# Optimization experiments

Measured on AMD Instinct MI355X. Metric: run time of the kernel, lower is better.

## Reference

```python
import jax, jax.numpy as jnp
import numpy as np

N, E, F_IN, H, C = 50000, 800000, 128, 4, 73
HC = H * C  # 292
NEG_SLOPE_ATT = 0.2   # GATv2 attention leaky relu
NEG_SLOPE_ACT = 0.01  # F.leaky_relu default
BN_EPS = 1e-5


def setup_inputs() -> dict:
    key = jax.random.key(0)
    ks = jax.random.split(key, 20)
    rn = lambda k, shp, s=0.05: (jax.random.normal(k, shp, jnp.float32) * s)
    inp = {
        'x': jax.random.normal(ks[0], (N, F_IN), jnp.float32),
        'edge_index': jax.random.randint(ks[1], (2, E), 0, N, jnp.int64),
        # conv1 (in=F_IN)
        'Wl1': rn(ks[2], (HC, F_IN)), 'bl1': rn(ks[3], (HC,)),
        'Wr1': rn(ks[4], (HC, F_IN)), 'br1': rn(ks[5], (HC,)),
        'att1': rn(ks[6], (H, C)), 'b1': rn(ks[7], (HC,)),
        # conv2 (in=HC)
        'Wl2': rn(ks[8], (HC, HC)), 'bl2': rn(ks[9], (HC,)),
        'Wr2': rn(ks[10], (HC, HC)), 'br2': rn(ks[11], (HC,)),
        'att2': rn(ks[12], (H, C)), 'b2': rn(ks[13], (HC,)),
        # shared BatchNorm1d(HC)
        'gamma': jnp.ones((HC,), jnp.float32), 'beta': jnp.zeros((HC,), jnp.float32),
        # classifier Linear(HC, 2)
        'Wc': rn(ks[14], (2, HC)), 'bc': rn(ks[15], (2,)),
    }
    return inp


def _gatv2(x, src, dst, Wl, bl, Wr, br, att, b):
    # lin_l on source, lin_r on target (PyG GATv2Conv, share_weights=False)
    xl = (x @ Wl.T + bl).reshape(-1, H, C)  # [N,H,C]
    xr = (x @ Wr.T + br).reshape(-1, H, C)
    f = xl[src] + xr[dst]                    # [E,H,C] edge-wise gather
    s = jnp.einsum('ehc,hc->eh', jax.nn.leaky_relu(f, NEG_SLOPE_ATT), att)
    # segment softmax over incoming edges of each destination node
    m = jax.ops.segment_max(s, dst, num_segments=N)
    ex = jnp.exp(s - m[dst])
    den = jax.ops.segment_sum(ex, dst, num_segments=N)
    alpha = ex / (den[dst] + 1e-16)          # [E,H]
    out = jax.ops.segment_sum(alpha[:, :, None] * xl[src], dst, num_segments=N)
    return out.reshape(-1, HC) + b           # concat heads + bias


def _bn(x, gamma, beta):
    mu = jnp.mean(x, axis=0)
    var = jnp.mean((x - mu) ** 2, axis=0)
    return (x - mu) * jax.lax.rsqrt(var + BN_EPS) * gamma + beta


def reference(x, edge_index, Wl1, bl1, Wr1, br1, att1, b1,
              Wl2, bl2, Wr2, br2, att2, b2, gamma, beta, Wc, bc):
    src, dst = edge_index[0], edge_index[1]
    h = _gatv2(x, src, dst, Wl1, bl1, Wr1, br1, att1, b1)
    h = jax.nn.leaky_relu(_bn(h, gamma, beta), NEG_SLOPE_ACT)
    h = _gatv2(h, src, dst, Wl2, bl2, Wr2, br2, att2, b2)
    h = jax.nn.leaky_relu(_bn(h, gamma, beta), NEG_SLOPE_ACT)
    return h @ Wc.T + bc
```

## Files before the change

### kernel.cpp

```cpp
#include <hip/hip_runtime.h>

#define HCDIM 292
#define NHEAD 4
#define CDIM 73
#define SLOTS 5
#define NPERM 320
#define BN_EPS 1e-5f
#define LOG2E 1.44269504f

using u16x8 = __attribute__((ext_vector_type(8))) unsigned short;
using f32x4 = __attribute__((ext_vector_type(4))) float;
using u16x4 = __attribute__((ext_vector_type(4))) unsigned short;
using hf2   = __attribute__((ext_vector_type(2))) _Float16;
using v2h   = __attribute__((ext_vector_type(2))) __fp16;
using v8h   = __attribute__((ext_vector_type(8))) __fp16;

__device__ inline v2h pkrtz(float a, float b) {
  return __builtin_amdgcn_cvt_pkrtz(a, b);
}
__device__ inline float fdot2(hf2 a, hf2 b, float c) {
  return __builtin_amdgcn_fdot2(__builtin_bit_cast(v2h, a),
                                __builtin_bit_cast(v2h, b), c, false);
}
__device__ inline ushort f2h(float f) {
  _Float16 h = (_Float16)f;
  return __builtin_bit_cast(ushort, h);
}
__device__ inline float h2f(ushort v) {
  return (float)__builtin_bit_cast(_Float16, v);
}
__device__ inline hf2 habs2(hf2 a) {
  unsigned u = __builtin_bit_cast(unsigned, a) & 0x7fff7fffu;
  return __builtin_bit_cast(hf2, u);
}
__device__ inline float fexp2(float x) {
  float r;
  asm("v_exp_f32 %0, %1" : "=v"(r) : "v"(x));
  return r;
}

#define FMAMIX_LO(ACC, W, U)                                                  \
  asm("v_fma_mix_f32 %0, %1, %2, %0 op_sel_hi:[1,0,0]"                        \
      : "+v"(ACC) : "v"(U), "v"(W))
#define FMAMIX_HI(ACC, W, U)                                                  \
  asm("v_fma_mix_f32 %0, %1, %2, %0 op_sel:[1,0,0] op_sel_hi:[1,0,0]"         \
      : "+v"(ACC) : "v"(U), "v"(W))

__device__ inline float dpp16_allsum(float v) {
  union { float f; int i; } a, b;
  a.f = v;
  b.i = __builtin_amdgcn_update_dpp(0, a.i, 0xB1, 0xf, 0xf, true);
  a.f += b.f;
  b.i = __builtin_amdgcn_update_dpp(0, a.i, 0x4E, 0xf, 0xf, true);
  a.f += b.f;
  b.i = __builtin_amdgcn_update_dpp(0, a.i, 0x124, 0xf, 0xf, true);
  a.f += b.f;
  b.i = __builtin_amdgcn_update_dpp(0, a.i, 0x128, 0xf, 0xf, true);
  a.f += b.f;
  return a.f;
}

__device__ inline int perm2feat(int p, bool& valid) {
  int h, c;
  if (p < 256) {
    h = p >> 6;
    c = ((p & 3) << 4) | ((p >> 2) & 15);
    valid = true;
  } else {
    int q = p - 256;
    h = q >> 4;
    c = 64 + (q & 15);
    valid = (q & 15) < (CDIM - 64);
  }
  return h * CDIM + c;
}

__global__ void k_wperm2(const float* __restrict__ W0, const float* __restrict__ b0,
                         const float* __restrict__ W1, const float* __restrict__ b1,
                         ushort* __restrict__ Wp, float* __restrict__ pb,
                         int Kin, int Kpad, int kperm,
                         const float* __restrict__ att1, const float* __restrict__ b1v,
                         const float* __restrict__ att2, const float* __restrict__ b2v,
                         const float* __restrict__ gamma, const float* __restrict__ beta,
                         const float* __restrict__ Wc, float* __restrict__ o) {
  int p = blockIdx.x, t = threadIdx.x;
  if (blockIdx.y == 2) {
    bool pv;
    int gn = perm2feat(p, pv);
    if (t < 8) {
      const float* src;
      switch (t) {
        case 0: src = att1; break;
        case 1: src = b1v; break;
        case 2: src = att2; break;
        case 3: src = b2v; break;
        case 4: src = gamma; break;
        case 5: src = beta; break;
        case 6: src = Wc; break;
        default: src = Wc + HCDIM; break;
      }
      o[t * NPERM + p] = pv ? src[gn] : 0.f;
    }
    return;
  }
  const float* W = blockIdx.y ? W1 : W0;
  const float* b = blockIdx.y ? b1 : b0;
  ushort* Wpo = Wp + (size_t)blockIdx.y * NPERM * Kpad;
  float* pbo = pb + blockIdx.y * NPERM;
  bool pv;
  int gn = perm2feat(p, pv);
  int gk = t;
  bool kv = t < Kin;
  if (kperm) { bool v2; gk = perm2feat(t, v2); kv = v2; }
  ushort v = 0;
  if (pv && kv) v = f2h(W[(size_t)gn * Kin + gk]);
  Wpo[(size_t)p * Kpad + t] = v;
  if (t == 0) pbo[p] = pv ? b[gn] : 0.f;
}

__global__ void k_hist(const int* __restrict__ dst, int* __restrict__ deg, int E) {
  int i = blockIdx.x * blockDim.x + threadIdx.x;
  int i4 = i * 4;
  if (i4 + 3 < E) {
    int4 d = *(const int4*)(dst + i4);
    atomicAdd(&deg[d.x], 1);
    atomicAdd(&deg[d.y], 1);
    atomicAdd(&deg[d.z], 1);
    atomicAdd(&deg[d.w], 1);
  } else {
    for (int k = i4; k < E; ++k) atomicAdd(&deg[dst[k]], 1);
  }
}

__global__ __launch_bounds__(256) void k_block_sum(const int* __restrict__ deg,
                                                   int* __restrict__ bsum, int n) {
  __shared__ int s[256];
  int i = blockIdx.x * 256 + threadIdx.x;
  s[threadIdx.x] = (i < n) ? deg[i] : 0;
  __syncthreads();
  for (int off = 128; off > 0; off >>= 1) {
    if (threadIdx.x < off) s[threadIdx.x] += s[threadIdx.x + off];
    __syncthreads();
  }
  if (threadIdx.x == 0) bsum[blockIdx.x] = s[0];
}

__global__ __launch_bounds__(256) void k_scan_small(const int* __restrict__ bsum,
                                                    int* __restrict__ boff, int G) {
  __shared__ int s[256];
  int t = threadIdx.x;
  int v = (t < G) ? bsum[t] : 0;
  s[t] = v;
  __syncthreads();
  for (int off = 1; off < 256; off <<= 1) {
    int tv = (t >= off) ? s[t - off] : 0;
    __syncthreads();
    s[t] += tv;
    __syncthreads();
  }
  if (t < G) boff[t] = s[t] - v;
}

__global__ __launch_bounds__(256) void k_scan_final(const int* __restrict__ deg,
                                                    const int* __restrict__ boff,
                                                    int* __restrict__ row_ptr,
                                                    int* __restrict__ cursor,
                                                    int n, int E) {
  __shared__ int s[256];
  int t = threadIdx.x;
  int i = blockIdx.x * 256 + t;
  int v = (i < n) ? deg[i] : 0;
  s[t] = v;
  __syncthreads();
  for (int off = 1; off < 256; off <<= 1) {
    int tv = (t >= off) ? s[t - off] : 0;
    __syncthreads();
    s[t] += tv;
    __syncthreads();
  }
  if (i < n) {
    int rp = boff[blockIdx.x] + s[t] - v;
    row_ptr[i] = rp;
    cursor[i] = rp;
  }
  if (i == 0) row_ptr[n] = E;
}

__global__ void k_csr_fill(const int* __restrict__ srcs, const int* __restrict__ dsts,
                           int* __restrict__ cursor, int* __restrict__ csr_src, int E) {
  int i = blockIdx.x * blockDim.x + threadIdx.x;
  int i4 = i * 4;
  if (i4 + 3 < E) {
    int4 s = *(const int4*)(srcs + i4);
    int4 d = *(const int4*)(dsts + i4);
    csr_src[atomicAdd(&cursor[d.x], 1)] = s.x;
    csr_src[atomicAdd(&cursor[d.y], 1)] = s.y;
    csr_src[atomicAdd(&cursor[d.z], 1)] = s.z;
    csr_src[atomicAdd(&cursor[d.w], 1)] = s.w;
  } else {
    for (int k = i4; k < E; ++k) {
      int pos = atomicAdd(&cursor[dsts[k]], 1);
      csr_src[pos] = srcs[k];
    }
  }
}

template <int KS, int MODE>
__global__ __launch_bounds__(256, 4) void k_gemm_a_lds(
    const void* __restrict__ Av, const ushort* __restrict__ Wb,
    const float* __restrict__ pb, const float* __restrict__ bnscale,
    const float* __restrict__ bnshift, ushort* __restrict__ o0,
    ushort* __restrict__ o1, int M) {
  constexpr int KSTEPS = KS / 32;
  constexpr int STR = KS + 8;
  __shared__ ushort As[64 * STR];
  const int tid = threadIdx.x;
  const int rbase = blockIdx.x * 64;
  const int wave = tid >> 6, lane = tid & 63;
  const int quad = lane >> 4, lr = lane & 15;
  const int ct = wave;

  if constexpr (MODE == 0) {
    const float* X = (const float*)Av;
    constexpr int NIT = (64 * KS / 16) / 256;
#pragma unroll
    for (int k = 0; k < NIT; ++k) {
      int idx = tid + k * 256;
      int row = idx >> 3, sg = idx & 7;
      int gr = rbase + row;
      if (gr >= M) gr = M - 1;
      const float4* p = (const float4*)(X + (size_t)gr * KS + sg * 16);
      float4 f0 = p[0], f1 = p[1], f2 = p[2], f3 = p[3];
      union { v2h h[4]; u16x8 v; } a, b;
      a.h[0] = pkrtz(f0.x, f0.y); a.h[1] = pkrtz(f0.z, f0.w);
      a.h[2] = pkrtz(f1.x, f1.y); a.h[3] = pkrtz(f1.z, f1.w);
      b.h[0] = pkrtz(f2.x, f2.y); b.h[1] = pkrtz(f2.z, f2.w);
      b.h[2] = pkrtz(f3.x, f3.y); b.h[3] = pkrtz(f3.z, f3.w);
      *(u16x8*)(As + row * STR + sg * 16) = a.v;
      *(u16x8*)(As + row * STR + sg * 16 + 8) = b.v;
    }
  } else {
    const ushort* Hn = (const ushort*)Av;
    constexpr int NIT = (64 * KS / 8) / 256;
#pragma unroll
    for (int k = 0; k < NIT; ++k) {
      int idx = tid + k * 256;
      int row = idx / (KS / 8), c8 = idx - row * (KS / 8);
      int gr = rbase + row;
      if (gr >= M) gr = M - 1;
      u16x8 v = *(const u16x8*)(Hn + (size_t)gr * KS + c8 * 8);
      int c = c8 * 8;
      float4 s0 = *(const float4*)(bnscale + c);
      float4 s1 = *(const float4*)(bnscale + c + 4);
      float4 t0 = *(const float4*)(bnshift + c);
      float4 t1 = *(const float4*)(bnshift + c + 4);
      float f[8];
      f[0] = fmaf(h2f(v[0]), s0.x, t0.x);
      f[1] = fmaf(h2f(v[1]), s0.y, t0.y);
      f[2] = fmaf(h2f(v[2]), s0.z, t0.z);
      f[3] = fmaf(h2f(v[3]), s0.w, t0.w);
      f[4] = fmaf(h2f(v[4]), s1.x, t1.x);
      f[5] = fmaf(h2f(v[5]), s1.y, t1.y);
      f[6] = fmaf(h2f(v[6]), s1.z, t1.z);
      f[7] = fmaf(h2f(v[7]), s1.w, t1.w);
#pragma unroll
      for (int j = 0; j < 8; ++j) f[j] = (f[j] > 0.f) ? f[j] : 0.01f * f[j];
      union { v2h h4[4]; u16x8 o; } u;
#pragma unroll
      for (int j = 0; j < 4; ++j) u.h4[j] = pkrtz(f[2 * j], f[2 * j + 1]);
      *(u16x8*)(As + row * STR + c8 * 8) = u.o;
    }
  }
  __syncthreads();

  const ushort* arow[4];
#pragma unroll
  for (int i = 0; i < 4; ++i) arow[i] = As + (i * 16 + lr) * STR;

#pragma unroll
  for (int y = 0; y < 2; ++y) {
    const ushort* bcol[5];
#pragma unroll
    for (int i = 0; i < 5; ++i)
      bcol[i] = Wb + (size_t)(y * 320 + ct * 80 + i * 16 + lr) * KS;

    f32x4 acc[4][5] = {};
#pragma unroll
    for (int s = 0; s < KSTEPS; ++s) {
      v8h bf[5], af[4];
#pragma unroll
      for (int i = 0; i < 5; ++i)
        bf[i] = *(const v8h*)(bcol[i] + s * 32 + quad * 8);
#pragma unroll
      for (int i = 0; i < 4; ++i)
        af[i] = *(const v8h*)(arow[i] + s * 32 + quad * 8);
#pragma unroll
      for (int ni = 0; ni < 5; ++ni)
#pragma unroll
        for (int mi = 0; mi < 4; ++mi)
          acc[mi][ni] = __builtin_amdgcn_mfma_f32_16x16x32_f16(
              bf[ni], af[mi], acc[mi][ni], 0, 0, 0);
    }

    ushort* out = y ? o1 : o0;
    const int colbase = ct * 80;
    float4 pbv[5];
#pragma unroll
    for (int ni = 0; ni < 5; ++ni)
      pbv[ni] = *(const float4*)(pb + y * 320 + ct * 80 + ni * 16 + quad * 4);
#pragma unroll
    for (int mi = 0; mi < 4; ++mi) {
      int gm = rbase + mi * 16 + lr;
      if (gm >= M) continue;
      ushort* orow = out + (size_t)gm * NPERM + colbase + quad * 4;
#pragma unroll
      for (int ni = 0; ni < 5; ++ni) {
        union { v2h h[2]; u16x4 o; } u;
        u.h[0] = pkrtz(acc[mi][ni][0] + pbv[ni].x, acc[mi][ni][1] + pbv[ni].y);
        u.h[1] = pkrtz(acc[mi][ni][2] + pbv[ni].z, acc[mi][ni][3] + pbv[ni].w);
        *(u16x4*)(orow + ni * 16) = u.o;
      }
    }
  }
}

__global__ __launch_bounds__(128) void k_agg(const ushort* __restrict__ xl,
                                             const ushort* __restrict__ xr,
                                             const int* __restrict__ csr_src,
                                             const int* __restrict__ row_ptr,
                                             const float* __restrict__ attp,
                                             const float* __restrict__ bp,
                                             ushort* __restrict__ out, int n) {
  int wave = threadIdx.x >> 6, lane = threadIdx.x & 63;
  int d = blockIdx.x * 2 + wave;
  if (d >= n) return;
  int start = __builtin_amdgcn_readfirstlane(row_ptr[d]);
  int end = __builtin_amdgcn_readfirstlane(row_ptr[d + 1]);

  float4 bp4 = *(const float4*)(bp + lane * 4);
  float bp5 = bp[256 + lane];

  if (start >= end) {
    union { v2h h[2]; u16x4 o; } u;
    u.h[0] = pkrtz(bp4.x, bp4.y);
    u.h[1] = pkrtz(bp4.z, bp4.w);
    *(u16x4*)(out + (size_t)d * NPERM + lane * 4) = u.o;
    out[(size_t)d * NPERM + 256 + lane] = f2h(bp5);
    return;
  }

  const float C = 0.4f * LOG2E;
  float4 at4 = *(const float4*)(attp + lane * 4);
  hf2 av01{(_Float16)(C * at4.x), (_Float16)(C * at4.y)};
  hf2 av23{(_Float16)(C * at4.z), (_Float16)(C * at4.w)};
  hf2 av5{(_Float16)(C * attp[256 + lane]), (_Float16)0.f};

  hf2 xr01, xr23, xr5;
  {
    uint2 rr = *(const uint2*)(xr + (size_t)d * NPERM + lane * 4);
    xr01 = __builtin_bit_cast(hf2, rr.x);
    xr23 = __builtin_bit_cast(hf2, rr.y);
    xr5 = hf2{__builtin_bit_cast(_Float16, xr[(size_t)d * NPERM + 256 + lane]),
              (_Float16)0.f};
  }
  float Tb = fdot2(xr01, av01, fdot2(xr23, av23, fdot2(xr5, av5, 0.f)));
  Tb = dpp16_allsum(Tb);
  float prv = 1.5f * Tb;
  float acc[SLOTS] = {};
  float den = 0.f;
  int dg = end - start;
  int nfull = dg >> 2;
  int rem = dg & 3;

  uint2 s8[4];
  ushort s1[4];
#pragma unroll
  for (int k = 0; k < 4; ++k) {
    int e = start + k;
    if (e > end - 1) e = end - 1;
    int s = __builtin_amdgcn_readfirstlane(csr_src[e]);
    s8[k] = *(const uint2*)(xl + (size_t)s * NPERM + lane * 4);
    s1[k] = xl[(size_t)s * NPERM + 256 + lane];
  }

  for (int g = 0; g < nfull; ++g) {
    int ebase = start + g * 4 + 4;
    uint2 n8[4];
    ushort n1[4];
#pragma unroll
    for (int k = 0; k < 4; ++k) {
      int e = ebase + k;
      if (e > end - 1) e = end - 1;
      int s = __builtin_amdgcn_readfirstlane(csr_src[e]);
      n8[k] = *(const uint2*)(xl + (size_t)s * NPERM + lane * 4);
      n1[k] = xl[(size_t)s * NPERM + 256 + lane];
    }

    float z[4];
#pragma unroll
    for (int k = 0; k < 4; ++k) {
      hf2 x01 = __builtin_bit_cast(hf2, s8[k].x);
      hf2 x23 = __builtin_bit_cast(hf2, s8[k].y);
      hf2 x5{__builtin_bit_cast(_Float16, s1[k]), (_Float16)0.f};
      float T = fdot2(habs2(x01 + xr01), av01,
                fdot2(habs2(x23 + xr23), av23,
                fdot2(habs2(x5 + xr5), av5, 0.f)));
      float Tl = fdot2(x01, av01, fdot2(x23, av23, fdot2(x5, av5, 0.f)));
      z[k] = fmaf(1.5f, Tl, T);
    }
#pragma unroll
    for (int k = 0; k < 4; ++k) z[k] = dpp16_allsum(z[k]);
    float w[4];
#pragma unroll
    for (int k = 0; k < 4; ++k) {
      w[k] = fexp2(fminf(z[k] + prv, 80.f));
      den += w[k];
    }
#pragma unroll
    for (int k = 0; k < 4; ++k) {
      unsigned ux = s8[k].x, uy = s8[k].y, u5 = (unsigned)s1[k];
      FMAMIX_LO(acc[0], w[k], ux);
      FMAMIX_HI(acc[1], w[k], ux);
      FMAMIX_LO(acc[2], w[k], uy);
      FMAMIX_HI(acc[3], w[k], uy);
      FMAMIX_LO(acc[4], w[k], u5);
    }
#pragma unroll
    for (int k = 0; k < 4; ++k) { s8[k] = n8[k]; s1[k] = n1[k]; }
  }

#pragma unroll
  for (int k = 0; k < 3; ++k) {
    if (k < rem) {
      hf2 x01 = __builtin_bit_cast(hf2, s8[k].x);
      hf2 x23 = __builtin_bit_cast(hf2, s8[k].y);
      hf2 x5{__builtin_bit_cast(_Float16, s1[k]), (_Float16)0.f};
      float T = fdot2(habs2(x01 + xr01), av01,
                fdot2(habs2(x23 + xr23), av23,
                fdot2(habs2(x5 + xr5), av5, 0.f)));
      float Tl = fdot2(x01, av01, fdot2(x23, av23, fdot2(x5, av5, 0.f)));
      float z = fmaf(1.5f, Tl, T);
      z = dpp16_allsum(z);
      float w = fexp2(fminf(z + prv, 80.f));
      den += w;
      unsigned ux = s8[k].x, uy = s8[k].y, u5 = (unsigned)s1[k];
      FMAMIX_LO(acc[0], w, ux);
      FMAMIX_HI(acc[1], w, ux);
      FMAMIX_LO(acc[2], w, uy);
      FMAMIX_HI(acc[3], w, uy);
      FMAMIX_LO(acc[4], w, u5);
    }
  }

  float inv = 1.f / (den + 1e-16f);
  union { v2h h[2]; u16x4 o; } u;
  u.h[0] = pkrtz(fmaf(acc[0], inv, bp4.x), fmaf(acc[1], inv, bp4.y));
  u.h[1] = pkrtz(fmaf(acc[2], inv, bp4.z), fmaf(acc[3], inv, bp4.w));
  *(u16x4*)(out + (size_t)d * NPERM + lane * 4) = u.o;
  out[(size_t)d * NPERM + 256 + lane] = f2h(fmaf(acc[4], inv, bp5));
}

__global__ __launch_bounds__(320) void k_bn_reduce(const ushort* __restrict__ h,
                                                   float* __restrict__ colsum,
                                                   float* __restrict__ colsq,
                                                   int n, int rows_per_block) {
  int c = threadIdx.x;
  int r0 = blockIdx.x * rows_per_block;
  int r1 = min(r0 + rows_per_block, n);
  float s = 0.f, s2 = 0.f;
  for (int r = r0; r < r1; ++r) {
    float v = h2f(h[(size_t)r * NPERM + c]);
    s += v;
    s2 += v * v;
  }
  atomicAdd(&colsum[c], s);
  atomicAdd(&colsq[c], s2);
}

__global__ void k_bn_coef(float* __restrict__ colsum, float* __restrict__ colsq,
                          const float* __restrict__ gp, const float* __restrict__ bp,
                          float invN) {
  int c = threadIdx.x + blockIdx.x * blockDim.x;
  if (c >= NPERM) return;
  float mu = colsum[c] * invN;
  float var = colsq[c] * invN - mu * mu;
  float scale = rsqrtf(var + BN_EPS) * gp[c];
  colsum[c] = scale;
  colsq[c] = bp[c] - mu * scale;
}

__global__ __launch_bounds__(256) void k_bn_classifier(
    const ushort* __restrict__ h, const float* __restrict__ scale,
    const float* __restrict__ shift, const float* __restrict__ wc0,
    const float* __restrict__ wc1, const float* __restrict__ bc,
    float* __restrict__ out, int n) {
  int wave = threadIdx.x >> 6, lane = threadIdx.x & 63;
  int r = blockIdx.x * 4 + wave;
  if (r >= n) return;
  float a0 = 0.f, a1 = 0.f;
#pragma unroll
  for (int k = 0; k < SLOTS; ++k) {
    int slot = lane + 64 * k;
    float v = fmaf(h2f(h[(size_t)r * NPERM + slot]), scale[slot], shift[slot]);
    v = (v > 0.f) ? v : 0.01f * v;
    a0 = fmaf(v, wc0[slot], a0);
    a1 = fmaf(v, wc1[slot], a1);
  }
#pragma unroll
  for (int off = 32; off > 0; off >>= 1) {
    a0 += __shfl_xor(a0, off, 64);
    a1 += __shfl_xor(a1, off, 64);
  }
  if (lane == 0) {
    out[(size_t)2 * r] = a0 + bc[0];
    out[(size_t)2 * r + 1] = a1 + bc[1];
  }
}

extern "C" void kernel_launch(void* const* d_in, const int* in_sizes, int n_in,
                              void* d_out, int out_size, void* d_ws, size_t ws_size,
                              hipStream_t stream) {
  const float* x      = (const float*)d_in[0];
  const int*   eidx   = (const int*)d_in[1];
  const float* Wl1    = (const float*)d_in[2];
  const float* bl1    = (const float*)d_in[3];
  const float* Wr1    = (const float*)d_in[4];
  const float* br1    = (const float*)d_in[5];
  const float* att1   = (const float*)d_in[6];
  const float* b1     = (const float*)d_in[7];
  const float* Wl2    = (const float*)d_in[8];
  const float* bl2    = (const float*)d_in[9];
  const float* Wr2    = (const float*)d_in[10];
  const float* br2    = (const float*)d_in[11];
  const float* att2   = (const float*)d_in[12];
  const float* b2     = (const float*)d_in[13];
  const float* gamma  = (const float*)d_in[14];
  const float* beta   = (const float*)d_in[15];
  const float* Wc     = (const float*)d_in[16];
  const float* bc     = (const float*)d_in[17];
  float* out = (float*)d_out;

  const int FIN = 128;
  const int N = in_sizes[0] / FIN;
  const int E = in_sizes[1] / 2;

  const int* src = eidx;
  const int* dst = eidx + E;

  ushort* h      = (ushort*)d_ws;
  ushort* xl     = h + (size_t)N * NPERM;
  ushort* xr     = xl + (size_t)N * NPERM;
  ushort* abuf   = xr + (size_t)N * NPERM;
  ushort* wb     = abuf + (size_t)N * NPERM;
  float* pb      = (float*)(wb + (size_t)2 * NPERM * NPERM);
  float* vecp    = pb + 2 * NPERM;
  float* pl      = vecp + 8 * NPERM;
  float* colsum  = pl + (size_t)N * NHEAD;
  float* colsq   = colsum + NPERM;
  int* deg       = (int*)(colsq + NPERM);
  int* row_ptr   = deg + N;
  int* cursor    = row_ptr + N + 1;
  int* bsum      = cursor + N;
  int* boff      = bsum + 256;
  int* csr_src   = boff + 256;

  const int G = (N + 255) / 256;
  const int EB4 = (E / 4 + 255) / 256;
  const int AGGB = (N + 3) / 4;
  const int AGG2 = (N + 1) / 2;
  const int GEMMB = (N + 63) / 64;

  const float* att1p = vecp;
  const float* b1p   = vecp + NPERM;
  const float* att2p = vecp + 2 * NPERM;
  const float* b2p   = vecp + 3 * NPERM;
  const float* gp    = vecp + 4 * NPERM;
  const float* btp   = vecp + 5 * NPERM;
  const float* wc0   = vecp + 6 * NPERM;
  const float* wc1   = vecp + 7 * NPERM;

  hipMemsetAsync(deg, 0, (size_t)N * sizeof(int), stream);
  k_hist<<<EB4, 256, 0, stream>>>(dst, deg, E);
  k_block_sum<<<G, 256, 0, stream>>>(deg, bsum, N);
  k_scan_small<<<1, 256, 0, stream>>>(bsum, boff, G);
  k_scan_final<<<G, 256, 0, stream>>>(deg, boff, row_ptr, cursor, N, E);
  k_csr_fill<<<EB4, 256, 0, stream>>>(src, dst, cursor, csr_src, E);

  k_wperm2<<<dim3(NPERM, 3), FIN, 0, stream>>>(Wl1, bl1, Wr1, br1, wb, pb,
                                               FIN, FIN, 0,
                                               att1, b1, att2, b2, gamma, beta,
                                               Wc, vecp);
  k_gemm_a_lds<128, 0><<<GEMMB, 256, 0, stream>>>((const void*)x, wb, pb,
                                                  nullptr, nullptr, xl, xr, N);
  k_agg<<<AGG2, 128, 0, stream>>>(xl, xr, csr_src, row_ptr, att1p, b1p, h, N);

  const int BNB = 1024;
  const int RPB = (N + BNB - 1) / BNB;
  hipMemsetAsync(colsum, 0, 2 * NPERM * sizeof(float), stream);
  k_bn_reduce<<<BNB, NPERM, 0, stream>>>(h, colsum, colsq, N, RPB);
  k_bn_coef<<<2, 160, 0, stream>>>(colsum, colsq, gp, btp, 1.f / (float)N);

  k_wperm2<<<dim3(NPERM, 2), NPERM, 0, stream>>>(Wl2, bl2, Wr2, br2, wb, pb,
                                                 HCDIM, NPERM, 1,
                                                 nullptr, nullptr, nullptr, nullptr,
                                                 nullptr, nullptr, nullptr, nullptr);
  k_gemm_a_lds<NPERM, 1><<<GEMMB, 256, 0, stream>>>((const void*)h, wb, pb,
                                                    colsum, colsq, xl, xr, N);
  k_agg<<<AGG2, 128, 0, stream>>>(xl, xr, csr_src, row_ptr, att2p, b2p, h, N);

  hipMemsetAsync(colsum, 0, 2 * NPERM * sizeof(float), stream);
  k_bn_reduce<<<BNB, NPERM, 0, stream>>>(h, colsum, colsq, N, RPB);
  k_bn_coef<<<2, 160, 0, stream>>>(colsum, colsq, gp, btp, 1.f / (float)N);

  k_bn_classifier<<<AGGB, 256, 0, stream>>>(h, colsum, colsq, wc0, wc1, bc, out, N);
}
```

Before: 547.4 us.

## Merge prep kernels, single-pass decoupled-lookback scan, fuse CSR fill and BN coef

Cuts the launch chain from about 16 dispatches to about 8. Weight permutation for both layers, parameter vector packing and the degree histogram now run in one k_prep kernel. The three-kernel scan becomes one single-pass decoupled-lookback scan, and the CSR fill runs as extra blocks of the first GEMM. The BN coefficient step moves into the last block of the reduction via a ticket counter, and the separate memsets are folded into one. The goal is less per-launch overhead and fewer idle gaps between kernels, at the cost of spin-waiting in the scan and a GEMM launch that mixes two unrelated workloads.

```diff
diff --git a/kernel.cpp b/kernel.cpp
--- a/kernel.cpp
+++ b/kernel.cpp
@@ -75,18 +75,38 @@
   return h * CDIM + c;
 }
 
-__global__ void k_wperm2(const float* __restrict__ W0, const float* __restrict__ b0,
-                         const float* __restrict__ W1, const float* __restrict__ b1,
-                         ushort* __restrict__ Wp, float* __restrict__ pb,
-                         int Kin, int Kpad, int kperm,
-                         const float* __restrict__ att1, const float* __restrict__ b1v,
-                         const float* __restrict__ att2, const float* __restrict__ b2v,
-                         const float* __restrict__ gamma, const float* __restrict__ beta,
-                         const float* __restrict__ Wc, float* __restrict__ o) {
-  int p = blockIdx.x, t = threadIdx.x;
-  if (blockIdx.y == 2) {
-    bool pv;
-    int gn = perm2feat(p, pv);
+__global__ __launch_bounds__(320) void k_prep(
+    const float* __restrict__ Wl1, const float* __restrict__ bl1,
+    const float* __restrict__ Wr1, const float* __restrict__ br1,
+    const float* __restrict__ Wl2, const float* __restrict__ bl2,
+    const float* __restrict__ Wr2, const float* __restrict__ br2,
+    ushort* __restrict__ wb1, float* __restrict__ pb1,
+    ushort* __restrict__ wb2, float* __restrict__ pb2,
+    const float* __restrict__ att1, const float* __restrict__ b1v,
+    const float* __restrict__ att2, const float* __restrict__ b2v,
+    const float* __restrict__ gamma, const float* __restrict__ beta,
+    const float* __restrict__ Wc, float* __restrict__ vecp,
+    const int* __restrict__ dst, int* __restrict__ deg, int E) {
+  int bx = blockIdx.x, t = threadIdx.x;
+  if (bx >= 5 * NPERM) {
+    int i = (bx - 5 * NPERM) * 320 + t;
+    int i4 = i * 4;
+    if (i4 + 3 < E) {
+      int4 d = *(const int4*)(dst + i4);
+      atomicAdd(&deg[d.x], 1);
+      atomicAdd(&deg[d.y], 1);
+      atomicAdd(&deg[d.z], 1);
+      atomicAdd(&deg[d.w], 1);
+    } else {
+      for (int k = i4; k < E; ++k) atomicAdd(&deg[dst[k]], 1);
+    }
+    return;
+  }
+  int seg = bx / NPERM;
+  int p = bx - seg * NPERM;
+  bool pv;
+  int gn = perm2feat(p, pv);
+  if (seg == 4) {
     if (t < 8) {
       const float* src;
       switch (t) {
@@ -99,76 +119,45 @@
         case 6: src = Wc; break;
         default: src = Wc + HCDIM; break;
       }
-      o[t * NPERM + p] = pv ? src[gn] : 0.f;
+      vecp[t * NPERM + p] = pv ? src[gn] : 0.f;
     }
     return;
   }
-  const float* W = blockIdx.y ? W1 : W0;
-  const float* b = blockIdx.y ? b1 : b0;
-  ushort* Wpo = Wp + (size_t)blockIdx.y * NPERM * Kpad;
-  float* pbo = pb + blockIdx.y * NPERM;
-  bool pv;
-  int gn = perm2feat(p, pv);
-  int gk = t;
-  bool kv = t < Kin;
-  if (kperm) { bool v2; gk = perm2feat(t, v2); kv = v2; }
-  ushort v = 0;
-  if (pv && kv) v = f2h(W[(size_t)gn * Kin + gk]);
-  Wpo[(size_t)p * Kpad + t] = v;
-  if (t == 0) pbo[p] = pv ? b[gn] : 0.f;
-}
-
-__global__ void k_hist(const int* __restrict__ dst, int* __restrict__ deg, int E) {
-  int i = blockIdx.x * blockDim.x + threadIdx.x;
-  int i4 = i * 4;
-  if (i4 + 3 < E) {
-    int4 d = *(const int4*)(dst + i4);
-    atomicAdd(&deg[d.x], 1);
-    atomicAdd(&deg[d.y], 1);
-    atomicAdd(&deg[d.z], 1);
-    atomicAdd(&deg[d.w], 1);
+  const float* W;
+  const float* b;
+  ushort* Wp;
+  float* pb;
+  int Kin, Kpad, kperm;
+  if (seg < 2) {
+    Kin = 128; Kpad = 128; kperm = 0;
+    W = seg ? Wr1 : Wl1; b = seg ? br1 : bl1;
+    Wp = wb1 + (size_t)seg * NPERM * 128; pb = pb1 + seg * NPERM;
   } else {
-    for (int k = i4; k < E; ++k) atomicAdd(&deg[dst[k]], 1);
-  }
-}
-
-__global__ __launch_bounds__(256) void k_block_sum(const int* __restrict__ deg,
-                                                   int* __restrict__ bsum, int n) {
+    Kin = HCDIM; Kpad = NPERM; kperm = 1;
+    int s2 = seg - 2;
+    W = s2 ? Wr2 : Wl2; b = s2 ? br2 : bl2;
+    Wp = wb2 + (size_t)s2 * NPERM * NPERM; pb = pb2 + s2 * NPERM;
+  }
+  if (t < Kpad) {
+    int gk = t;
+    bool kv = t < Kin;
+    if (kperm) { bool v2; gk = perm2feat(t, v2); kv = v2; }
+    ushort v = 0;
+    if (pv && kv) v = f2h(W[(size_t)gn * Kin + gk]);
+    Wp[(size_t)p * Kpad + t] = v;
+  }
+  if (t == 0) pb[p] = pv ? b[gn] : 0.f;
+}
+
+__global__ __launch_bounds__(256) void k_scan_lb(const int* __restrict__ deg,
+                                                 unsigned* __restrict__ st,
+                                                 int* __restrict__ row_ptr,
+                                                 int* __restrict__ cursor,
+                                                 int n, int E) {
   __shared__ int s[256];
-  int i = blockIdx.x * 256 + threadIdx.x;
-  s[threadIdx.x] = (i < n) ? deg[i] : 0;
-  __syncthreads();
-  for (int off = 128; off > 0; off >>= 1) {
-    if (threadIdx.x < off) s[threadIdx.x] += s[threadIdx.x + off];
-    __syncthreads();
-  }
-  if (threadIdx.x == 0) bsum[blockIdx.x] = s[0];
-}
-
-__global__ __launch_bounds__(256) void k_scan_small(const int* __restrict__ bsum,
-                                                    int* __restrict__ boff, int G) {
-  __shared__ int s[256];
-  int t = threadIdx.x;
-  int v = (t < G) ? bsum[t] : 0;
-  s[t] = v;
-  __syncthreads();
-  for (int off = 1; off < 256; off <<= 1) {
-    int tv = (t >= off) ? s[t - off] : 0;
-    __syncthreads();
-    s[t] += tv;
-    __syncthreads();
-  }
-  if (t < G) boff[t] = s[t] - v;
-}
-
-__global__ __launch_bounds__(256) void k_scan_final(const int* __restrict__ deg,
-                                                    const int* __restrict__ boff,
-                                                    int* __restrict__ row_ptr,
-                                                    int* __restrict__ cursor,
-                                                    int n, int E) {
-  __shared__ int s[256];
-  int t = threadIdx.x;
-  int i = blockIdx.x * 256 + t;
+  __shared__ int sprefix;
+  int bid = blockIdx.x, t = threadIdx.x;
+  int i = bid * 256 + t;
   int v = (i < n) ? deg[i] : 0;
   s[t] = v;
   __syncthreads();
@@ -178,39 +167,62 @@
     s[t] += tv;
     __syncthreads();
   }
+  if (t == 0) {
+    unsigned total = (unsigned)s[255];
+    __hip_atomic_store(&st[bid], (1u << 30) | total, __ATOMIC_RELEASE,
+                       __HIP_MEMORY_SCOPE_AGENT);
+    unsigned run = 0;
+    int p = bid - 1;
+    while (p >= 0) {
+      unsigned x;
+      do {
+        x = __hip_atomic_load(&st[p], __ATOMIC_ACQUIRE, __HIP_MEMORY_SCOPE_AGENT);
+        if (x == 0u) __builtin_amdgcn_s_sleep(1);
+      } while (x == 0u);
+      run += x & 0x3FFFFFFFu;
+      if ((x >> 30) == 2u) break;
+      --p;
+    }
+    __hip_atomic_store(&st[bid], (2u << 30) | (run + total), __ATOMIC_RELEASE,
+                       __HIP_MEMORY_SCOPE_AGENT);
+    sprefix = (int)run;
+  }
+  __syncthreads();
+  int run = sprefix;
   if (i < n) {
-    int rp = boff[blockIdx.x] + s[t] - v;
+    int rp = run + s[t] - v;
     row_ptr[i] = rp;
     cursor[i] = rp;
   }
   if (i == 0) row_ptr[n] = E;
 }
 
-__global__ void k_csr_fill(const int* __restrict__ srcs, const int* __restrict__ dsts,
-                           int* __restrict__ cursor, int* __restrict__ csr_src, int E) {
-  int i = blockIdx.x * blockDim.x + threadIdx.x;
-  int i4 = i * 4;
-  if (i4 + 3 < E) {
-    int4 s = *(const int4*)(srcs + i4);
-    int4 d = *(const int4*)(dsts + i4);
-    csr_src[atomicAdd(&cursor[d.x], 1)] = s.x;
-    csr_src[atomicAdd(&cursor[d.y], 1)] = s.y;
-    csr_src[atomicAdd(&cursor[d.z], 1)] = s.z;
-    csr_src[atomicAdd(&cursor[d.w], 1)] = s.w;
-  } else {
-    for (int k = i4; k < E; ++k) {
-      int pos = atomicAdd(&cursor[dsts[k]], 1);
-      csr_src[pos] = srcs[k];
-    }
-  }
-}
-
-template <int KS, int MODE>
+template <int KS, int MODE, int FILL>
 __global__ __launch_bounds__(256, 4) void k_gemm_a_lds(
     const void* __restrict__ Av, const ushort* __restrict__ Wb,
     const float* __restrict__ pb, const float* __restrict__ bnscale,
     const float* __restrict__ bnshift, ushort* __restrict__ o0,
-    ushort* __restrict__ o1, int M) {
+    ushort* __restrict__ o1, int M,
+    const int* __restrict__ srcs, const int* __restrict__ dsts,
+    int* __restrict__ cursor, int* __restrict__ csr_src, int E, int gemmb) {
+  if (FILL && (int)blockIdx.x >= gemmb) {
+    int i = ((int)blockIdx.x - gemmb) * 256 + (int)threadIdx.x;
+    int i4 = i * 4;
+    if (i4 + 3 < E) {
+      int4 s = *(const int4*)(srcs + i4);
+      int4 d = *(const int4*)(dsts + i4);
+      csr_src[atomicAdd(&cursor[d.x], 1)] = s.x;
+      csr_src[atomicAdd(&cursor[d.y], 1)] = s.y;
+      csr_src[atomicAdd(&cursor[d.z], 1)] = s.z;
+      csr_src[atomicAdd(&cursor[d.w], 1)] = s.w;
+    } else {
+      for (int k = i4; k < E; ++k) {
+        int pos = atomicAdd(&cursor[dsts[k]], 1);
+        csr_src[pos] = srcs[k];
+      }
+    }
+    return;
+  }
   constexpr int KSTEPS = KS / 32;
   constexpr int STR = KS + 8;
   __shared__ ushort As[64 * STR];
@@ -460,10 +472,11 @@
   out[(size_t)d * NPERM + 256 + lane] = f2h(fmaf(acc[4], inv, bp5));
 }
 
-__global__ __launch_bounds__(320) void k_bn_reduce(const ushort* __restrict__ h,
-                                                   float* __restrict__ colsum,
-                                                   float* __restrict__ colsq,
-                                                   int n, int rows_per_block) {
+__global__ __launch_bounds__(320) void k_bn_reduce_f(
+    const ushort* __restrict__ h, float* __restrict__ colsum,
+    float* __restrict__ colsq, int* __restrict__ ticket,
+    const float* __restrict__ gp, const float* __restrict__ bp,
+    int n, int rows_per_block, float invN, int nblocks) {
   int c = threadIdx.x;
   int r0 = blockIdx.x * rows_per_block;
   int r1 = min(r0 + rows_per_block, n);
@@ -475,18 +488,23 @@
   }
   atomicAdd(&colsum[c], s);
   atomicAdd(&colsq[c], s2);
-}
-
-__global__ void k_bn_coef(float* __restrict__ colsum, float* __restrict__ colsq,
-                          const float* __restrict__ gp, const float* __restrict__ bp,
-                          float invN) {
-  int c = threadIdx.x + blockIdx.x * blockDim.x;
-  if (c >= NPERM) return;
-  float mu = colsum[c] * invN;
-  float var = colsq[c] * invN - mu * mu;
-  float scale = rsqrtf(var + BN_EPS) * gp[c];
-  colsum[c] = scale;
-  colsq[c] = bp[c] - mu * scale;
+  __threadfence();
+  __syncthreads();
+  __shared__ int lastf;
+  if (c == 0) lastf = (atomicAdd(ticket, 1) == nblocks - 1) ? 1 : 0;
+  __syncthreads();
+  if (lastf) {
+    __threadfence();
+    float sum = __hip_atomic_load(&colsum[c], __ATOMIC_RELAXED,
+                                  __HIP_MEMORY_SCOPE_AGENT);
+    float sq = __hip_atomic_load(&colsq[c], __ATOMIC_RELAXED,
+                                 __HIP_MEMORY_SCOPE_AGENT);
+    float mu = sum * invN;
+    float var = sq * invN - mu * mu;
+    float scale = rsqrtf(var + BN_EPS) * gp[c];
+    colsum[c] = scale;
+    colsq[c] = bp[c] - mu * scale;
+  }
 }
 
 __global__ __launch_bounds__(256) void k_bn_classifier(
@@ -550,25 +568,29 @@
   ushort* h      = (ushort*)d_ws;
   ushort* xl     = h + (size_t)N * NPERM;
   ushort* xr     = xl + (size_t)N * NPERM;
-  ushort* abuf   = xr + (size_t)N * NPERM;
-  ushort* wb     = abuf + (size_t)N * NPERM;
-  float* pb      = (float*)(wb + (size_t)2 * NPERM * NPERM);
-  float* vecp    = pb + 2 * NPERM;
-  float* pl      = vecp + 8 * NPERM;
-  float* colsum  = pl + (size_t)N * NHEAD;
-  float* colsq   = colsum + NPERM;
-  int* deg       = (int*)(colsq + NPERM);
-  int* row_ptr   = deg + N;
+  ushort* wb1    = xr + (size_t)N * NPERM;
+  ushort* wb2    = wb1 + (size_t)2 * NPERM * 128;
+  float* pb1     = (float*)(wb2 + (size_t)2 * NPERM * NPERM);
+  float* pb2     = pb1 + 2 * NPERM;
+  float* vecp    = pb2 + 2 * NPERM;
+  int* row_ptr   = (int*)(vecp + 8 * NPERM);
   int* cursor    = row_ptr + N + 1;
-  int* bsum      = cursor + N;
-  int* boff      = bsum + 256;
-  int* csr_src   = boff + 256;
+  int* csr_src   = cursor + N;
+  int* deg       = csr_src + E;
+  unsigned* scanst = (unsigned*)(deg + N);
+  int* tickets   = (int*)(scanst + 256);
+  float* colsum1 = (float*)(tickets + 4);
+  float* colsq1  = colsum1 + NPERM;
+  float* colsum2 = colsq1 + NPERM;
+  float* colsq2  = colsum2 + NPERM;
+  const size_t zero_bytes = (size_t)(N + 256 + 4 + 4 * NPERM) * 4;
 
   const int G = (N + 255) / 256;
-  const int EB4 = (E / 4 + 255) / 256;
   const int AGGB = (N + 3) / 4;
   const int AGG2 = (N + 1) / 2;
   const int GEMMB = (N + 63) / 64;
+  const int FB = (E + 1023) / 1024;
+  const int HISTB = (E + 1279) / 1280;
 
   const float* att1p = vecp;
   const float* b1p   = vecp + NPERM;
@@ -579,38 +601,26 @@
   const float* wc0   = vecp + 6 * NPERM;
   const float* wc1   = vecp + 7 * NPERM;
 
-  hipMemsetAsync(deg, 0, (size_t)N * sizeof(int), stream);
-  k_hist<<<EB4, 256, 0, stream>>>(dst, deg, E);
-  k_block_sum<<<G, 256, 0, stream>>>(deg, bsum, N);
-  k_scan_small<<<1, 256, 0, stream>>>(bsum, boff, G);
-  k_scan_final<<<G, 256, 0, stream>>>(deg, boff, row_ptr, cursor, N, E);
-  k_csr_fill<<<EB4, 256, 0, stream>>>(src, dst, cursor, csr_src, E);
-
-  k_wperm2<<<dim3(NPERM, 3), FIN, 0, stream>>>(Wl1, bl1, Wr1, br1, wb, pb,
-                                               FIN, FIN, 0,
-                                               att1, b1, att2, b2, gamma, beta,
-                                               Wc, vecp);
-  k_gemm_a_lds<128, 0><<<GEMMB, 256, 0, stream>>>((const void*)x, wb, pb,
-                                                  nullptr, nullptr, xl, xr, N);
-  k_agg<<<AGG2, 128, 0, stream>>>(xl, xr, csr_src, row_ptr, att1p, b1p, h, N);
-
   const int BNB = 1024;
   const int RPB = (N + BNB - 1) / BNB;
-  hipMemsetAsync(colsum, 0, 2 * NPERM * sizeof(float), stream);
-  k_bn_reduce<<<BNB, NPERM, 0, stream>>>(h, colsum, colsq, N, RPB);
-  k_bn_coef<<<2, 160, 0, stream>>>(colsum, colsq, gp, btp, 1.f / (float)N);
-
-  k_wperm2<<<dim3(NPERM, 2), NPERM, 0, stream>>>(Wl2, bl2, Wr2, br2, wb, pb,
-                                                 HCDIM, NPERM, 1,
-                                                 nullptr, nullptr, nullptr, nullptr,
-                                                 nullptr, nullptr, nullptr, nullptr);
-  k_gemm_a_lds<NPERM, 1><<<GEMMB, 256, 0, stream>>>((const void*)h, wb, pb,
-                                                    colsum, colsq, xl, xr, N);
+
+  hipMemsetAsync(deg, 0, zero_bytes, stream);
+  k_prep<<<5 * NPERM + HISTB, 320, 0, stream>>>(
+      Wl1, bl1, Wr1, br1, Wl2, bl2, Wr2, br2, wb1, pb1, wb2, pb2,
+      att1, b1, att2, b2, gamma, beta, Wc, vecp, dst, deg, E);
+  k_scan_lb<<<G, 256, 0, stream>>>(deg, scanst, row_ptr, cursor, N, E);
+  k_gemm_a_lds<128, 0, 1><<<GEMMB + FB, 256, 0, stream>>>(
+      (const void*)x, wb1, pb1, nullptr, nullptr, xl, xr, N,
+      src, dst, cursor, csr_src, E, GEMMB);
+  k_agg<<<AGG2, 128, 0, stream>>>(xl, xr, csr_src, row_ptr, att1p, b1p, h, N);
+  k_bn_reduce_f<<<BNB, NPERM, 0, stream>>>(h, colsum1, colsq1, &tickets[0],
+                                           gp, btp, N, RPB, 1.f / (float)N, BNB);
+  k_gemm_a_lds<NPERM, 1, 0><<<GEMMB, 256, 0, stream>>>(
+      (const void*)h, wb2, pb2, colsum1, colsq1, xl, xr, N,
+      nullptr, nullptr, nullptr, nullptr, 0, GEMMB);
   k_agg<<<AGG2, 128, 0, stream>>>(xl, xr, csr_src, row_ptr, att2p, b2p, h, N);
-
-  hipMemsetAsync(colsum, 0, 2 * NPERM * sizeof(float), stream);
-  k_bn_reduce<<<BNB, NPERM, 0, stream>>>(h, colsum, colsq, N, RPB);
-  k_bn_coef<<<2, 160, 0, stream>>>(colsum, colsq, gp, btp, 1.f / (float)N);
-
-  k_bn_classifier<<<AGGB, 256, 0, stream>>>(h, colsum, colsq, wc0, wc1, bc, out, N);
-}
+  k_bn_reduce_f<<<BNB, NPERM, 0, stream>>>(h, colsum2, colsq2, &tickets[1],
+                                           gp, btp, N, RPB, 1.f / (float)N, BNB);
+  k_bn_classifier<<<AGGB, 256, 0, stream>>>(h, colsum2, colsq2, wc0, wc1, bc,
+                                            out, N);
+}
```

Measured after the change: 668.8 us. 1.22x slower.
